# Kernel tuning notes

Hardware: AMD Instinct MI355X
Metric: run time of the kernel (lower is better)

The kernel has to match this reference:

```python
import jax, jax.numpy as jnp
import numpy as np

KB, KI = 6, 0   # kernel quantizer: quantized_bits(6, 0, alpha=1)
BB, BI = 6, 0   # bias quantizer:   quantized_bits(6, 0, alpha=1)
AB, AI = 6, 0   # activation:       quantized_relu(6, 0)


def _round_ste(p):
    # straight-through round (QKeras _round_through); tf.round and jnp.round
    # both round half-to-even
    return p + jax.lax.stop_gradient(jnp.round(p) - p)


def quantized_bits(x, bits, integer):
    # QKeras quantized_bits with keep_negative=1, symmetric=0, alpha=1
    m = float(2 ** (bits - 1))      # non-sign levels
    m_i = float(2 ** integer)
    p = x * (m / m_i)
    return (m_i / m) * jnp.clip(_round_ste(p), -m, m - 1.0)


def quantized_relu(x, bits, integer):
    # QKeras quantized_relu with negative_slope=0, use_sigmoid=0
    m = float(2 ** bits)
    m_i = float(2 ** integer)
    p = x * (m / m_i)
    return (m_i / m) * jnp.clip(_round_ste(p), 0.0, m - 1.0)


def setup_inputs() -> dict:
    key = jax.random.key(0)
    ks = jax.random.split(key, 9)
    dims = [128, 1024, 2048, 4096, 4096]
    inp = {"x": jax.random.normal(ks[0], (8192, dims[0]), dtype=jnp.float32)}
    for i in range(4):
        fan_in, fan_out = dims[i], dims[i + 1]
        scale = np.sqrt(2.0 / (fan_in + fan_out))  # glorot-ish scale
        inp[f"W{i}"] = jax.random.normal(ks[1 + 2 * i], (fan_in, fan_out), dtype=jnp.float32) * scale
        inp[f"b{i}"] = jax.random.normal(ks[2 + 2 * i], (fan_out,), dtype=jnp.float32) * 0.01
    return inp


def reference(x, W0, b0, W1, b1, W2, b2, W3, b3):
    Ws = [W0, W1, W2, W3]
    bs = [b0, b1, b2, b3]
    h = x
    for i in range(4):
        wq = quantized_bits(Ws[i], KB, KI)
        bq = quantized_bits(bs[i], BB, BI)
        h = jnp.dot(h, wq) + bq
        if i != 3:  # last layer has activation=None
            h = quantized_relu(h, AB, AI)
    return h
```

## Files before the change

### kernel.cpp

```cpp
#include <hip/hip_runtime.h>
#include <stdint.h>

typedef int v4i __attribute__((ext_vector_type(4)));

__device__ __forceinline__ float qlevel(float x) {
  float p = rintf(x * 32.0f);
  return fminf(fmaxf(p, -32.0f), 31.0f);
}

__device__ __forceinline__ int8_t qrelu_level(float p) {
  int q = (int)rintf(p);
  q = q < 0 ? 0 : (q > 63 ? 63 : q);
  return (int8_t)q;
}

__device__ __forceinline__ void async16(const void* g, void* l) {
  __builtin_amdgcn_global_load_lds(
      (const __attribute__((address_space(1))) void*)g,
      (__attribute__((address_space(3))) void*)l, 16, 0, 0);
}

__global__ __launch_bounds__(256) void quant_w0_k(const float* __restrict__ W,
                                                  int8_t* __restrict__ wq) {
  int i = blockIdx.x * 256 + threadIdx.x;
  float4 v = ((const float4*)W)[i];
  char4 c;
  c.x = (int8_t)(int)qlevel(v.x);
  c.y = (int8_t)(int)qlevel(v.y);
  c.z = (int8_t)(int)qlevel(v.z);
  c.w = (int8_t)(int)qlevel(v.w);
  ((char4*)wq)[i] = c;
}

__global__ __launch_bounds__(256) void quantT_k(const float* __restrict__ W,
                                                int8_t* __restrict__ wt,
                                                int K, int N) {
  const int t = threadIdx.x;
  const int l = t & 63;
  const int kc = t >> 6;
  const int k0 = blockIdx.y * 64 + kc * 16;
  const int n = blockIdx.x * 64 + l;
  union { int8_t b[16]; int4 v; } u;
#pragma unroll
  for (int j = 0; j < 16; ++j)
    u.b[j] = (int8_t)(int)qlevel(W[(size_t)(k0 + j) * N + n]);
  *(int4*)&wt[(size_t)n * K + k0] = u.v;
}

__global__ __launch_bounds__(256) void quant_bias_k(
    const float* __restrict__ b0, const float* __restrict__ b1,
    const float* __restrict__ b2, const float* __restrict__ b3,
    float* __restrict__ o0, float* __restrict__ o1,
    float* __restrict__ o2, float* __restrict__ o3) {
  int i = blockIdx.x * 256 + threadIdx.x;
  if (i < 1024) o0[i] = qlevel(b0[i]);
  if (i < 2048) o1[i] = qlevel(b1[i]);
  o2[i] = qlevel(b2[i]);
  o3[i] = qlevel(b3[i]);
}

__global__ __launch_bounds__(256) void layer0_k(const float* __restrict__ x,
                                                const int8_t* __restrict__ w0q,
                                                const float* __restrict__ bint,
                                                int8_t* __restrict__ a1) {
  const int K = 128, N = 1024;
  __shared__ float xs[64][132];
  __shared__ int8_t wsm[128][64];
  const int tid = threadIdx.x;
  const int m0 = blockIdx.y * 64;
  const int n0 = blockIdx.x * 64;
#pragma unroll
  for (int i = 0; i < 8; ++i) {
    int idx = tid + 256 * i;
    int row = idx >> 5, c4 = idx & 31;
    float4 v = *(const float4*)(x + (size_t)(m0 + row) * K + c4 * 4);
    *(float4*)&xs[row][c4 * 4] = v;
  }
#pragma unroll
  for (int i = 0; i < 8; ++i) {
    int idx = tid + 256 * i;
    int k = idx >> 4, c4 = idx & 15;
    *(int*)&wsm[k][c4 * 4] = *(const int*)(w0q + (size_t)k * N + n0 + c4 * 4);
  }
  __syncthreads();
  const int ty = tid >> 4, tx = tid & 15;
  float acc[4][4] = {};
  for (int k4 = 0; k4 < K; k4 += 4) {
    float xr[4][4];
#pragma unroll
    for (int i = 0; i < 4; ++i) {
      float4 v = *(const float4*)&xs[ty * 4 + i][k4];
      xr[i][0] = v.x; xr[i][1] = v.y; xr[i][2] = v.z; xr[i][3] = v.w;
    }
#pragma unroll
    for (int kk = 0; kk < 4; ++kk) {
      char4 cv = *(const char4*)&wsm[k4 + kk][tx * 4];
      float w0 = (float)cv.x, w1 = (float)cv.y, w2 = (float)cv.z, w3 = (float)cv.w;
#pragma unroll
      for (int i = 0; i < 4; ++i) {
        acc[i][0] = fmaf(xr[i][kk], w0, acc[i][0]);
        acc[i][1] = fmaf(xr[i][kk], w1, acc[i][1]);
        acc[i][2] = fmaf(xr[i][kk], w2, acc[i][2]);
        acc[i][3] = fmaf(xr[i][kk], w3, acc[i][3]);
      }
    }
  }
  const int n = n0 + tx * 4;
  float b0v = 2.0f * bint[n + 0], b1v = 2.0f * bint[n + 1];
  float b2v = 2.0f * bint[n + 2], b3v = 2.0f * bint[n + 3];
#pragma unroll
  for (int i = 0; i < 4; ++i) {
    int m = m0 + ty * 4 + i;
    char4 o;
    o.x = qrelu_level(2.0f * acc[i][0] + b0v);
    o.y = qrelu_level(2.0f * acc[i][1] + b1v);
    o.z = qrelu_level(2.0f * acc[i][2] + b2v);
    o.w = qrelu_level(2.0f * acc[i][3] + b3v);
    *(char4*)&a1[(size_t)m * 1024 + n] = o;
  }
}

template <bool FINAL>
__global__ __launch_bounds__(512) void gemm_i8(const int8_t* __restrict__ A,
                                               const int8_t* __restrict__ BT,
                                               const float* __restrict__ bint,
                                               void* __restrict__ outp,
                                               int M, int N, int K) {
  __shared__ __align__(16) int8_t ldsA[4][256 * 64];
  __shared__ __align__(16) int8_t ldsB[4][256 * 64];
  const int tid = threadIdx.x;
  const int wid = tid >> 6;
  const int lane = tid & 63;
  const int wm = wid >> 2, wn = wid & 3;
  const int quad = lane >> 4, r = lane & 15;
  const int m0 = blockIdx.y * 256, n0 = blockIdx.x * 256;

  const int8_t* Ab = A + (size_t)m0 * K;
  const int8_t* Bb = BT + (size_t)n0 * K;

  const int srow = tid >> 2;
  const int sp = tid & 3;
  const int skc = (sp - (srow >> 1)) & 3;
  const int8_t* gA0 = Ab + (size_t)srow * K + skc * 16;
  const int8_t* gA1 = Ab + (size_t)(srow + 128) * K + skc * 16;
  const int8_t* gB0 = Bb + (size_t)srow * K + skc * 16;
  const int8_t* gB1 = Bb + (size_t)(srow + 128) * K + skc * 16;
  const int ldsOff0 = (wid * 64) * 16;
  const int ldsOff1 = (512 + wid * 64) * 16;

  const int pfrag = (quad + (r >> 1)) & 3;

  v4i acc[8][4] = {};

#define STAGE(buf, kt)                                   \
  do {                                                   \
    const int koff_ = (kt) * 64;                         \
    async16(gA0 + koff_, &ldsA[buf][ldsOff0]);           \
    async16(gA1 + koff_, &ldsA[buf][ldsOff1]);           \
    async16(gB0 + koff_, &ldsB[buf][ldsOff0]);           \
    async16(gB1 + koff_, &ldsB[buf][ldsOff1]);           \
  } while (0)

#define COMPUTE(pbuf)                                                         \
  do {                                                                        \
    const int8_t* La_ = &ldsA[pbuf][0];                                       \
    const int8_t* Lb_ = &ldsB[pbuf][0];                                       \
    v4i bf[4], af[4];                                                         \
    _Pragma("unroll")                                                         \
    for (int nt = 0; nt < 4; ++nt)                                            \
      bf[nt] = *(const v4i*)&Lb_[(wn * 64 + nt * 16 + r) * 64 + pfrag * 16];  \
    _Pragma("unroll")                                                         \
    for (int mt = 0; mt < 4; ++mt)                                            \
      af[mt] = *(const v4i*)&La_[(wm * 128 + mt * 16 + r) * 64 + pfrag * 16]; \
    __builtin_amdgcn_s_setprio(1);                                            \
    _Pragma("unroll")                                                         \
    for (int mt = 0; mt < 4; ++mt)                                            \
      _Pragma("unroll")                                                       \
      for (int nt = 0; nt < 4; ++nt)                                          \
        acc[mt][nt] = __builtin_amdgcn_mfma_i32_16x16x64_i8(                  \
            af[mt], bf[nt], acc[mt][nt], 0, 0, 0);                            \
    __builtin_amdgcn_s_setprio(0);                                            \
    _Pragma("unroll")                                                         \
    for (int mt = 0; mt < 4; ++mt)                                            \
      af[mt] = *(const v4i*)&La_[(wm * 128 + 64 + mt * 16 + r) * 64 +         \
                                 pfrag * 16];                                 \
    __builtin_amdgcn_s_setprio(1);                                            \
    _Pragma("unroll")                                                         \
    for (int mt = 0; mt < 4; ++mt)                                            \
      _Pragma("unroll")                                                       \
      for (int nt = 0; nt < 4; ++nt)                                          \
        acc[4 + mt][nt] = __builtin_amdgcn_mfma_i32_16x16x64_i8(              \
            af[mt], bf[nt], acc[4 + mt][nt], 0, 0, 0);                        \
    __builtin_amdgcn_s_setprio(0);                                            \
  } while (0)

  const int NT = K >> 6;

  STAGE(0, 0);
  STAGE(1, 1);
  STAGE(2, 2);
  STAGE(3, 3);
  asm volatile("s_waitcnt vmcnt(12)" ::: "memory");
  __builtin_amdgcn_s_barrier();

  for (int t = 0; t < NT - 4; ++t) {
    const int p = t & 3;
    COMPUTE(p);
    __builtin_amdgcn_s_barrier();
    STAGE(p, t + 4);
    asm volatile("s_waitcnt vmcnt(12)" ::: "memory");
    __builtin_amdgcn_s_barrier();
  }
  COMPUTE((NT - 4) & 3);
  asm volatile("s_waitcnt vmcnt(8)" ::: "memory");
  __builtin_amdgcn_s_barrier();
  COMPUTE((NT - 3) & 3);
  asm volatile("s_waitcnt vmcnt(4)" ::: "memory");
  __builtin_amdgcn_s_barrier();
  COMPUTE((NT - 2) & 3);
  asm volatile("s_waitcnt vmcnt(0)" ::: "memory");
  __builtin_amdgcn_s_barrier();
  COMPUTE((NT - 1) & 3);

#undef STAGE
#undef COMPUTE

  const int mbase = m0 + wm * 128;
  const int nbase = n0 + wn * 64;
  if (FINAL) {
    float* out = (float*)outp;
#pragma unroll
    for (int nt = 0; nt < 4; ++nt) {
      int n = nbase + nt * 16 + r;
      float bq = bint[n] * 0.03125f;
#pragma unroll
      for (int mt = 0; mt < 8; ++mt)
#pragma unroll
        for (int g = 0; g < 4; ++g) {
          int m = mbase + mt * 16 + quad * 4 + g;
          out[(size_t)m * N + n] = (float)acc[mt][nt][g] * (1.0f / 2048.0f) + bq;
        }
    }
  } else {
    int8_t* out = (int8_t*)outp;
#pragma unroll
    for (int nt = 0; nt < 4; ++nt) {
      int n = nbase + nt * 16 + r;
      float b2 = 2.0f * bint[n];
#pragma unroll
      for (int mt = 0; mt < 8; ++mt)
#pragma unroll
        for (int g = 0; g < 4; ++g) {
          int m = mbase + mt * 16 + quad * 4 + g;
          out[(size_t)m * N + n] =
              qrelu_level((float)acc[mt][nt][g] * 0.03125f + b2);
        }
    }
  }
}

extern "C" void kernel_launch(void* const* d_in, const int* in_sizes, int n_in,
                              void* d_out, int out_size, void* d_ws, size_t ws_size,
                              hipStream_t stream) {
  const float* x  = (const float*)d_in[0];
  const float* W0 = (const float*)d_in[1];
  const float* b0 = (const float*)d_in[2];
  const float* W1 = (const float*)d_in[3];
  const float* b1 = (const float*)d_in[4];
  const float* W2 = (const float*)d_in[5];
  const float* b2 = (const float*)d_in[6];
  const float* W3 = (const float*)d_in[7];
  const float* b3 = (const float*)d_in[8];

  uint8_t* ws = (uint8_t*)d_ws;
  int8_t* wq0 = (int8_t*)(ws + 0);
  int8_t* wt1 = (int8_t*)(ws + 131072);
  int8_t* wt2 = (int8_t*)(ws + 2228224);
  int8_t* wt3 = (int8_t*)(ws + 10616832);
  float*  bq0 = (float*)(ws + 27394048);
  float*  bq1 = (float*)(ws + 27398144);
  float*  bq2 = (float*)(ws + 27406336);
  float*  bq3 = (float*)(ws + 27422720);
  int8_t* a1  = (int8_t*)(ws + 27439104);
  int8_t* a2  = (int8_t*)(ws + 35827712);
  int8_t* a3  = (int8_t*)(ws + 52604928);

  quant_w0_k<<<128, 256, 0, stream>>>(W0, wq0);
  quantT_k<<<dim3(2048 / 64, 1024 / 64), 256, 0, stream>>>(W1, wt1, 1024, 2048);
  quantT_k<<<dim3(4096 / 64, 2048 / 64), 256, 0, stream>>>(W2, wt2, 2048, 4096);
  quantT_k<<<dim3(4096 / 64, 4096 / 64), 256, 0, stream>>>(W3, wt3, 4096, 4096);
  quant_bias_k<<<16, 256, 0, stream>>>(b0, b1, b2, b3, bq0, bq1, bq2, bq3);
  layer0_k<<<dim3(16, 128), 256, 0, stream>>>(x, wq0, bq0, a1);
  gemm_i8<false><<<dim3(2048 / 256, 8192 / 256), 512, 0, stream>>>(
      a1, wt1, bq1, a2, 8192, 2048, 1024);
  gemm_i8<false><<<dim3(4096 / 256, 8192 / 256), 512, 0, stream>>>(
      a2, wt2, bq2, a3, 8192, 4096, 2048);
  gemm_i8<true><<<dim3(4096 / 256, 8192 / 256), 512, 0, stream>>>(
      a3, wt3, bq3, d_out, 8192, 4096, 4096);
}
```

Baseline: 539.2 us.

## Restructure int8 GEMM pipeline to triple-buffered LDS with interleaved A/B staging

Reduces the LDS ring from four to three stages per operand and splits each k-tile's global-to-LDS loads into A and B halves. The halves are issued between the two MFMA half-iterations, with barriers and sched_barriers fencing each compute phase. This cuts LDS use per block (128KB to 96KB) and spreads memory traffic across the loop. In exchange it shortens prefetch depth and adds several barriers per iteration, which may expose load latency or stall waves.

```diff
diff --git a/kernel.cpp b/kernel.cpp
--- a/kernel.cpp
+++ b/kernel.cpp
@@ -126,8 +126,8 @@
                                                const float* __restrict__ bint,
                                                void* __restrict__ outp,
                                                int M, int N, int K) {
-  __shared__ __align__(16) int8_t ldsA[4][256 * 64];
-  __shared__ __align__(16) int8_t ldsB[4][256 * 64];
+  __shared__ __align__(16) int8_t ldsA[3][256 * 64];
+  __shared__ __align__(16) int8_t ldsB[3][256 * 64];
   const int tid = threadIdx.x;
   const int wid = tid >> 6;
   const int lane = tid & 63;
@@ -152,26 +152,32 @@
 
   v4i acc[8][4] = {};
 
-#define STAGE(buf, kt)                                   \
-  do {                                                   \
-    const int koff_ = (kt) * 64;                         \
-    async16(gA0 + koff_, &ldsA[buf][ldsOff0]);           \
-    async16(gA1 + koff_, &ldsA[buf][ldsOff1]);           \
-    async16(gB0 + koff_, &ldsB[buf][ldsOff0]);           \
-    async16(gB1 + koff_, &ldsB[buf][ldsOff1]);           \
+#define STAGE_A(buf, kt)                              \
+  do {                                                \
+    async16(gA0 + (kt) * 64, &ldsA[buf][ldsOff0]);    \
+    async16(gA1 + (kt) * 64, &ldsA[buf][ldsOff1]);    \
   } while (0)
-
-#define COMPUTE(pbuf)                                                         \
+#define STAGE_B(buf, kt)                              \
+  do {                                                \
+    async16(gB0 + (kt) * 64, &ldsB[buf][ldsOff0]);    \
+    async16(gB1 + (kt) * 64, &ldsB[buf][ldsOff1]);    \
+  } while (0)
+
+#define ITER(p, q, kt, doStage, vmN)                                          \
   do {                                                                        \
-    const int8_t* La_ = &ldsA[pbuf][0];                                       \
-    const int8_t* Lb_ = &ldsB[pbuf][0];                                       \
     v4i bf[4], af[4];                                                         \
+    const int8_t* La_ = &ldsA[p][0];                                          \
+    const int8_t* Lb_ = &ldsB[p][0];                                          \
     _Pragma("unroll")                                                         \
     for (int nt = 0; nt < 4; ++nt)                                            \
       bf[nt] = *(const v4i*)&Lb_[(wn * 64 + nt * 16 + r) * 64 + pfrag * 16];  \
     _Pragma("unroll")                                                         \
     for (int mt = 0; mt < 4; ++mt)                                            \
       af[mt] = *(const v4i*)&La_[(wm * 128 + mt * 16 + r) * 64 + pfrag * 16]; \
+    if (doStage) STAGE_A(q, kt);                                              \
+    __builtin_amdgcn_s_barrier();                                             \
+    asm volatile("s_waitcnt lgkmcnt(0)" ::: "memory");                        \
+    __builtin_amdgcn_sched_barrier(0);                                        \
     __builtin_amdgcn_s_setprio(1);                                            \
     _Pragma("unroll")                                                         \
     for (int mt = 0; mt < 4; ++mt)                                            \
@@ -180,10 +186,17 @@
         acc[mt][nt] = __builtin_amdgcn_mfma_i32_16x16x64_i8(                  \
             af[mt], bf[nt], acc[mt][nt], 0, 0, 0);                            \
     __builtin_amdgcn_s_setprio(0);                                            \
+    __builtin_amdgcn_s_barrier();                                             \
     _Pragma("unroll")                                                         \
     for (int mt = 0; mt < 4; ++mt)                                            \
       af[mt] = *(const v4i*)&La_[(wm * 128 + 64 + mt * 16 + r) * 64 +         \
                                  pfrag * 16];                                 \
+    if (doStage) STAGE_B(q, kt);                                              \
+    if (vmN == 4) asm volatile("s_waitcnt vmcnt(4)" ::: "memory");            \
+    if (vmN == 0) asm volatile("s_waitcnt vmcnt(0)" ::: "memory");            \
+    __builtin_amdgcn_s_barrier();                                             \
+    asm volatile("s_waitcnt lgkmcnt(0)" ::: "memory");                        \
+    __builtin_amdgcn_sched_barrier(0);                                        \
     __builtin_amdgcn_s_setprio(1);                                            \
     _Pragma("unroll")                                                         \
     for (int mt = 0; mt < 4; ++mt)                                            \
@@ -192,38 +205,25 @@
         acc[4 + mt][nt] = __builtin_amdgcn_mfma_i32_16x16x64_i8(              \
             af[mt], bf[nt], acc[4 + mt][nt], 0, 0, 0);                        \
     __builtin_amdgcn_s_setprio(0);                                            \
+    __builtin_amdgcn_s_barrier();                                             \
   } while (0)
 
   const int NT = K >> 6;
 
-  STAGE(0, 0);
-  STAGE(1, 1);
-  STAGE(2, 2);
-  STAGE(3, 3);
-  asm volatile("s_waitcnt vmcnt(12)" ::: "memory");
-  __builtin_amdgcn_s_barrier();
-
-  for (int t = 0; t < NT - 4; ++t) {
-    const int p = t & 3;
-    COMPUTE(p);
-    __builtin_amdgcn_s_barrier();
-    STAGE(p, t + 4);
-    asm volatile("s_waitcnt vmcnt(12)" ::: "memory");
-    __builtin_amdgcn_s_barrier();
-  }
-  COMPUTE((NT - 4) & 3);
-  asm volatile("s_waitcnt vmcnt(8)" ::: "memory");
-  __builtin_amdgcn_s_barrier();
-  COMPUTE((NT - 3) & 3);
+  STAGE_A(0, 0); STAGE_B(0, 0);
+  STAGE_A(1, 1); STAGE_B(1, 1);
   asm volatile("s_waitcnt vmcnt(4)" ::: "memory");
   __builtin_amdgcn_s_barrier();
-  COMPUTE((NT - 2) & 3);
-  asm volatile("s_waitcnt vmcnt(0)" ::: "memory");
-  __builtin_amdgcn_s_barrier();
-  COMPUTE((NT - 1) & 3);
-
-#undef STAGE
-#undef COMPUTE
+
+  for (int t = 0; t < NT - 2; ++t) {
+    ITER(t % 3, (t + 2) % 3, t + 2, true, 4);
+  }
+  ITER((NT - 2) % 3, 0, 0, false, 0);
+  ITER((NT - 1) % 3, 0, 0, false, -1);
+
+#undef ITER
+#undef STAGE_A
+#undef STAGE_B
 
   const int mbase = m0 + wm * 128;
   const int nbase = n0 + wn * 64;
```

Result: faster. 492.6 us (-8.6%).
